# Performance work log

Measured on AMD Instinct MI355X. Metric: run time of the kernel, lower is better.

Reference implementation:

```python
import jax, jax.numpy as jnp
import numpy as np

N_LAYERS = 4
D_IN = 64
D_OUT = 64
D_MODEL = 512
D_STATE = 256
RMIN, RMAX, MAX_PHASE = 0.8, 0.95, 2.0 * np.pi


def setup_inputs() -> dict:
    key = jax.random.key(0)
    rng = np.random.default_rng(0)
    B, L = 8, 2048
    u = jax.random.normal(key, (B, L, D_IN), dtype=jnp.float32)
    # encoder/decoder (nn.Linear, bias=False): weight shape [out, in]
    encoder_w = jnp.asarray(rng.standard_normal((D_MODEL, D_IN)) / np.sqrt(D_IN), jnp.float32)
    decoder_w = jnp.asarray(rng.standard_normal((D_OUT, D_MODEL)) / np.sqrt(D_MODEL), jnp.float32)
    # LRU params per block (standard ring init on eigenvalues)
    u1 = rng.uniform(size=(N_LAYERS, D_STATE))
    u2 = rng.uniform(size=(N_LAYERS, D_STATE))
    nu_log = jnp.asarray(np.log(-0.5 * np.log(u1 * (RMAX**2 - RMIN**2) + RMIN**2)), jnp.float32)
    theta_log = jnp.asarray(np.log(MAX_PHASE * u2), jnp.float32)
    B_re = jnp.asarray(rng.standard_normal((N_LAYERS, D_STATE, D_MODEL)) / np.sqrt(2 * D_MODEL), jnp.float32)
    B_im = jnp.asarray(rng.standard_normal((N_LAYERS, D_STATE, D_MODEL)) / np.sqrt(2 * D_MODEL), jnp.float32)
    C_re = jnp.asarray(rng.standard_normal((N_LAYERS, D_MODEL, D_STATE)) / np.sqrt(D_STATE), jnp.float32)
    C_im = jnp.asarray(rng.standard_normal((N_LAYERS, D_MODEL, D_STATE)) / np.sqrt(D_STATE), jnp.float32)
    D = jnp.asarray(rng.standard_normal((N_LAYERS, D_MODEL)), jnp.float32)
    # GLU feedforward: y = (x W1^T) * sigmoid(x W2^T)
    W1 = jnp.asarray(rng.standard_normal((N_LAYERS, D_MODEL, D_MODEL)) / np.sqrt(D_MODEL), jnp.float32)
    W2 = jnp.asarray(rng.standard_normal((N_LAYERS, D_MODEL, D_MODEL)) / np.sqrt(D_MODEL), jnp.float32)
    res_logit = jnp.full((N_LAYERS,), -1.0, jnp.float32)
    return dict(u=u, encoder_w=encoder_w, decoder_w=decoder_w, nu_log=nu_log,
                theta_log=theta_log, B_re=B_re, B_im=B_im, C_re=C_re, C_im=C_im,
                D=D, W1=W1, W2=W2, res_logit=res_logit)


def _lru(x, nu, th, Bre, Bim, Cre, Cim, Dv):
    # diagonal complex LRU: h_t = lam*h_{t-1} + gamma*B u_t ; y = Re(C h) + D*u
    lam = jnp.exp(-jnp.exp(nu) + 1j * jnp.exp(th)).astype(jnp.complex64)  # [N]
    gam = jnp.sqrt(1.0 - jnp.abs(lam) ** 2).astype(jnp.complex64)
    Bc = (Bre + 1j * Bim).astype(jnp.complex64)  # [N, D]
    Bu = jnp.einsum('bld,nd->bln', x.astype(jnp.complex64), Bc) * gam  # [B,L,N]
    lam_b = jnp.broadcast_to(lam, Bu.shape)

    def comb(a, b):
        return (a[0] * b[0], a[1] * b[0] + b[1])

    _, h = jax.lax.associative_scan(comb, (lam_b, Bu), axis=1)
    Cc = (Cre + 1j * Cim).astype(jnp.complex64)  # [D, N]
    return jnp.real(jnp.einsum('bln,dn->bld', h, Cc)) + Dv * x


def reference(u, encoder_w, decoder_w, nu_log, theta_log, B_re, B_im, C_re, C_im, D, W1, W2, res_logit):
    x = jnp.einsum('bli,mi->blm', u, encoder_w)  # encoder
    for k in range(N_LAYERS):
        z = _lru(x, nu_log[k], theta_log[k], B_re[k], B_im[k], C_re[k], C_im[k], D[k])
        z = jnp.einsum('bld,od->blo', z, W1[k]) * jax.nn.sigmoid(jnp.einsum('bld,od->blo', z, W2[k]))
        x = x + jax.nn.sigmoid(res_logit[k]) * z  # gated residual (dropout=0)
    return jnp.einsum('blm,om->blo', x, decoder_w)  # decoder
```

## Files before the change

kernel.cpp:

```cpp
#include <hip/hip_runtime.h>
#include <cmath>

#define DM 512
#define DS 256
#define NL 4
#define BATCH 8
#define SEQ 2048
#define MROWS (BATCH*SEQ)
#define LCH 32
#define NCH 64

typedef unsigned short ushort_t;
typedef unsigned int uint_t;
typedef __attribute__((ext_vector_type(8))) short short8;
typedef __attribute__((ext_vector_type(4))) float floatx4;

__device__ __forceinline__ float sigmoidf_(float v) { return 1.0f / (1.0f + __expf(-v)); }

__device__ __forceinline__ ushort_t f2bf(float f) {
    union { float f; unsigned int u; } c; c.f = f;
    unsigned int u = c.u;
    u += 0x7fffu + ((u >> 16) & 1u);
    return (ushort_t)(u >> 16);
}
__device__ __forceinline__ float bf2f(uint_t h) {
    union { unsigned int u; float f; } c; c.u = (h & 0xffffu) << 16; return c.f;
}
__device__ __forceinline__ uint_t pack2(float a, float b) {
    return (uint_t)f2bf(a) | ((uint_t)f2bf(b) << 16);
}

#define AS1 __attribute__((address_space(1)))
#define AS3 __attribute__((address_space(3)))
__device__ __forceinline__ void gl_lds16(const void* g, void* l) {
    __builtin_amdgcn_global_load_lds((const AS1 uint_t*)g, (AS3 uint_t*)l, 16, 0, 0);
}

struct GemmArgs {
    const ushort_t* A;
    const ushort_t* Wa;
    const ushort_t* Wb;
    const ushort_t* xbf_in;
    const float* gam;
    const float* Dv;
    float* of32;
    ushort_t* obf;
    const float* resp;
    const float* lamre;
    const float* lamim;
    float* carry;
    int K;
    int N;
    int layer;
};

#define PREFETCH_TILE(it_, buf_)                                                        \
    do {                                                                                \
        const size_t kb_ = (size_t)(it_) * 64;                                          \
        char* dst_ = smem + (buf_) * HALF;                                              \
        gl_lds16(Ap + (size_t)(wid * 16 + lrow) * Kb + kb_, dst_ + wid * 1024);         \
        gl_lds16(Ap + (size_t)((wid + 4) * 16 + lrow) * Kb + kb_,                       \
                 dst_ + (wid + 4) * 1024);                                              \
        gl_lds16(B0p + (size_t)(wid * 16 + lrow) * Kb + kb_, dst_ + AB + wid * 1024);   \
        if constexpr (BN == 128) {                                                      \
            gl_lds16(B0p + (size_t)((wid + 4) * 16 + lrow) * Kb + kb_,                  \
                     dst_ + AB + (wid + 4) * 1024);                                     \
        }                                                                               \
        if constexpr (DUAL) {                                                           \
            gl_lds16(B1p + (size_t)(wid * 16 + lrow) * Kb + kb_,                        \
                     dst_ + AB + BB + wid * 1024);                                      \
            if constexpr (BN == 128) {                                                  \
                gl_lds16(B1p + (size_t)((wid + 4) * 16 + lrow) * Kb + kb_,              \
                         dst_ + AB + BB + (wid + 4) * 1024);                            \
            }                                                                           \
        }                                                                               \
    } while (0)

template<int BN, int EPI, int DUAL>
__launch_bounds__(256, DUAL ? 2 : 3)
__global__ void mgemm(const GemmArgs p) {
    constexpr int BM = 128;
    constexpr int MT = (BN == 128) ? 4 : 2;
    constexpr int NT = 4;
    constexpr int WROWS = MT * 16;
    constexpr int AB = 8192;
    constexpr int BB = (BN == 128) ? 8192 : 4096;
    constexpr int B1B = DUAL ? BB : 0;
    constexpr int HALF = AB + BB + B1B;
    constexpr int EPB = (EPI == 4) ? 0
                      : (EPI == 1) ? (32 * 132 * 4 + 128 * 66 * 4)
                      : 32 * 132 * 4;
    constexpr int SMB = (2 * HALF > EPB) ? 2 * HALF : EPB;
    __shared__ __align__(16) char smem[SMB];

    const int K = p.K, N = p.N;
    const int tid = threadIdx.x, lane = tid & 63, wid = tid >> 6;
    const int wm = (BN == 128) ? (wid & 1) : wid;
    const int wn = (BN == 128) ? (wid >> 1) : 0;
    const int m0 = blockIdx.x * BM, n0 = blockIdx.y * BN;
    const int q = lane >> 4, r16 = lane & 15;
    const int lrow = lane >> 2;
    const size_t Kb = (size_t)K * 2;
    const char* Ap  = (const char*)p.A  + (size_t)m0 * Kb + (lane & 3) * 16;
    const char* B0p = (const char*)p.Wa + (size_t)n0 * Kb + (lane & 3) * 16;
    const char* B1p = (const char*)p.Wb + (size_t)n0 * Kb + (lane & 3) * 16;

    floatx4 acc0[MT][NT] = {};
    floatx4 acc1[DUAL ? MT : 1][DUAL ? NT : 1] = {};

    const int iters = K >> 5;
    PREFETCH_TILE(0, 0);
    for (int it = 0; it < iters; ++it) {
        __syncthreads();
        if (it + 1 < iters) PREFETCH_TILE(it + 1, (it + 1) & 1);
        const ushort_t* As  = (const ushort_t*)(smem + (it & 1) * HALF);
        const ushort_t* Bs0 = (const ushort_t*)(smem + (it & 1) * HALF + AB);
        const ushort_t* Bs1 = (const ushort_t*)(smem + (it & 1) * HALF + AB + BB);

        short8 af[MT], b0[NT], b1[DUAL ? NT : 1];
#pragma unroll
        for (int i = 0; i < MT; ++i)
            af[i] = *(const short8*)&As[(wm * WROWS + i * 16 + r16) * 32 + q * 8];
#pragma unroll
        for (int j = 0; j < NT; ++j) {
            b0[j] = *(const short8*)&Bs0[(wn * 64 + j * 16 + r16) * 32 + q * 8];
            if constexpr (DUAL)
                b1[j] = *(const short8*)&Bs1[(wn * 64 + j * 16 + r16) * 32 + q * 8];
        }
#pragma unroll
        for (int i = 0; i < MT; ++i)
#pragma unroll
            for (int j = 0; j < NT; ++j) {
                acc0[i][j] = __builtin_amdgcn_mfma_f32_16x16x32_bf16(af[i], b0[j], acc0[i][j], 0, 0, 0);
                if constexpr (DUAL)
                    acc1[i][j] = __builtin_amdgcn_mfma_f32_16x16x32_bf16(af[i], b1[j], acc1[i][j], 0, 0, 0);
            }
    }

    if constexpr (EPI == 4) {
#pragma unroll
        for (int i = 0; i < MT; ++i)
#pragma unroll
            for (int j = 0; j < NT; ++j)
#pragma unroll
                for (int rr = 0; rr < 4; ++rr) {
                    const int row = m0 + wm * WROWS + i * 16 + q * 4 + rr;
                    const int col = wn * 64 + j * 16 + r16;
                    p.of32[(size_t)row * N + col] = acc0[i][j][rr];
                }
        return;
    } else {
        float* eps = (float*)smem;
        uint_t* zst = (uint_t*)(smem + 32 * 132 * 4);
        float rsv = 0.f;
        if constexpr (EPI == 3) rsv = sigmoidf_(p.resp[p.layer]);

#pragma unroll
        for (int i = 0; i < MT; ++i) {
            __syncthreads();
#pragma unroll
            for (int j = 0; j < NT; ++j) {
                const int colt = wn * 64 + j * 16 + r16;
#pragma unroll
                for (int rr = 0; rr < 4; ++rr) {
                    float v = acc0[i][j][rr];
                    if constexpr (EPI == 1) v *= p.gam[(n0 + colt) >> 1];
                    if constexpr (EPI == 3) v = rsv * v * sigmoidf_(acc1[i][j][rr]);
                    eps[(wm * 16 + q * 4 + rr) * 132 + colt] = v;
                }
            }
            __syncthreads();
            const int row_r = tid >> 3, colg = (tid & 7) * 16;
            const int lr = (row_r >> 4) * 64 + i * 16 + (row_r & 15);
            const int grow = m0 + lr;
            const int gcol = n0 + colg;
            float4 f[4];
#pragma unroll
            for (int c = 0; c < 4; ++c) f[c] = *(float4*)&eps[row_r * 132 + colg + c * 4];
            const size_t ob = (size_t)grow * N + gcol;

            if constexpr (EPI == 2) {
                uint_t xp[8];
                *(uint4*)(xp)     = *(const uint4*)(p.xbf_in + ob);
                *(uint4*)(xp + 4) = *(const uint4*)(p.xbf_in + ob + 8);
#pragma unroll
                for (int c = 0; c < 4; ++c) {
                    float4 dv = *(const float4*)(p.Dv + gcol + c * 4);
                    f[c].x += dv.x * bf2f(xp[2 * c]);
                    f[c].y += dv.y * bf2f(xp[2 * c] >> 16);
                    f[c].z += dv.z * bf2f(xp[2 * c + 1]);
                    f[c].w += dv.w * bf2f(xp[2 * c + 1] >> 16);
                }
            } else if constexpr (EPI == 3) {
                uint_t xp[8];
                *(uint4*)(xp)     = *(const uint4*)(p.xbf_in + ob);
                *(uint4*)(xp + 4) = *(const uint4*)(p.xbf_in + ob + 8);
#pragma unroll
                for (int c = 0; c < 4; ++c) {
                    f[c].x += bf2f(xp[2 * c]);
                    f[c].y += bf2f(xp[2 * c] >> 16);
                    f[c].z += bf2f(xp[2 * c + 1]);
                    f[c].w += bf2f(xp[2 * c + 1] >> 16);
                }
            }
            uint4 p0, p1;
            p0.x = pack2(f[0].x, f[0].y); p0.y = pack2(f[0].z, f[0].w);
            p0.z = pack2(f[1].x, f[1].y); p0.w = pack2(f[1].z, f[1].w);
            p1.x = pack2(f[2].x, f[2].y); p1.y = pack2(f[2].z, f[2].w);
            p1.z = pack2(f[3].x, f[3].y); p1.w = pack2(f[3].z, f[3].w);
            *(uint4*)(p.obf + ob) = p0;
            *(uint4*)(p.obf + ob + 8) = p1;
            if constexpr (EPI == 1) {
                const int c0 = colg >> 1;
                *(uint4*)&zst[lr * 66 + c0]     = p0;
                *(uint4*)&zst[lr * 66 + c0 + 4] = p1;
            }
        }

        if constexpr (EPI == 1) {
            __syncthreads();
            const int c4 = tid >> 6, s6 = tid & 63;
            const int sg = (n0 >> 1) + s6;
            const float lr_ = p.lamre[sg], li_ = p.lamim[sg];
            float hr = 0.f, hi = 0.f;
#pragma unroll 8
            for (int i2 = 0; i2 < LCH; ++i2) {
                uint_t uu = zst[(c4 * LCH + i2) * 66 + s6];
                float br = bf2f(uu), bi = bf2f(uu >> 16);
                float nr = fmaf(lr_, hr, fmaf(-li_, hi, br));
                float ni = fmaf(lr_, hi, fmaf(li_, hr, bi));
                hr = nr; hi = ni;
            }
            const int b = m0 >> 11;
            const int cblk = ((m0 & (SEQ - 1)) >> 5) + c4;
            const size_t cb = (size_t)(b * NCH + cblk) * 512 + sg;
            p.carry[cb] = hr; p.carry[cb + DS] = hi;
        }
    }
}

__global__ void prep_all(const float* __restrict__ u, const float* __restrict__ enc,
                         const float* __restrict__ dec, const float* __restrict__ nu,
                         const float* __restrict__ th,
                         const float* __restrict__ Bre, const float* __restrict__ Bim,
                         const float* __restrict__ Cre, const float* __restrict__ Cim,
                         const float* __restrict__ W1, const float* __restrict__ W2,
                         ushort_t* __restrict__ WBb, ushort_t* __restrict__ Wzb,
                         ushort_t* __restrict__ W1b, ushort_t* __restrict__ W2b,
                         ushort_t* __restrict__ encb, ushort_t* __restrict__ decb,
                         ushort_t* __restrict__ ubf,
                         float* __restrict__ lre, float* __restrict__ lim,
                         float* __restrict__ gm) {
    const int idx = blockIdx.x * 256 + threadIdx.x;
    const int k = idx & 511, n = (idx >> 9) & 511, l = idx >> 18;
    {
        const int s = n >> 1, part = n & 1;
        const float* src = part ? Bim : Bre;
        WBb[idx] = f2bf(src[((size_t)l * DS + s) * DM + k]);
    }
    {
        const int s = k >> 1, part = k & 1;
        float v = part ? -Cim[((size_t)l * DM + n) * DS + s]
                       :  Cre[((size_t)l * DM + n) * DS + s];
        Wzb[idx] = f2bf(v);
    }
    W1b[idx] = f2bf(W1[idx]);
    W2b[idx] = f2bf(W2[idx]);
    ubf[idx] = f2bf(u[idx]);
    if (idx < DM * 64) { encb[idx] = f2bf(enc[idx]); decb[idx] = f2bf(dec[idx]); }
    if (idx < NL * DS) {
        float a = expf(-expf(nu[idx])), t = expf(th[idx]);
        lre[idx] = a * cosf(t);
        lim[idx] = a * sinf(t);
        gm[idx] = sqrtf(fmaxf(0.f, 1.f - a * a));
    }
}

__global__ __launch_bounds__(256) void scan_apply_lb(
        const uint_t* __restrict__ Bu, const float* __restrict__ lre_,
        const float* __restrict__ lim_, const float* __restrict__ carry,
        uint_t* __restrict__ h) {
    const int s = threadIdx.x;
    const int blk = blockIdx.x, b = blk >> 6, c = blk & 63;
    const float lre = lre_[s], lim = lim_[s];

    float gre = 0.f, gim = 0.f;
    if (c > 0) {
        float are = lre, aim = lim;
#pragma unroll
        for (int t = 0; t < 5; ++t) {
            float nr = are * are - aim * aim, ni = 2.f * are * aim;
            are = nr; aim = ni;
        }
        const int depth = (c < 12) ? c : 12;
        float pwr = 1.f, pwi = 0.f;
        for (int j = c - 1; j >= c - depth; --j) {
            const size_t jb = (size_t)(b * NCH + j) * 512 + s;
            float er = carry[jb], ei = carry[jb + DS];
            gre = fmaf(pwr, er, fmaf(-pwi, ei, gre));
            gim = fmaf(pwr, ei, fmaf(pwi, er, gim));
            float nr = pwr * are - pwi * aim, ni = pwr * aim + pwi * are;
            pwr = nr; pwi = ni;
        }
    }

    float hr = gre, hi = gim;
    size_t base = ((size_t)b * SEQ + (size_t)c * LCH) * DS + s;
#pragma unroll 8
    for (int i = 0; i < LCH; ++i, base += DS) {
        uint_t uu = Bu[base];
        float br = bf2f(uu), bi = bf2f(uu >> 16);
        float nr = fmaf(lre, hr, fmaf(-lim, hi, br));
        float ni = fmaf(lre, hi, fmaf(lim, hr, bi));
        hr = nr; hi = ni;
        h[base] = pack2(hr, hi);
    }
}

extern "C" void kernel_launch(void* const* d_in, const int* in_sizes, int n_in,
                              void* d_out, int out_size, void* d_ws, size_t ws_size,
                              hipStream_t stream) {
    const float* u   = (const float*)d_in[0];
    const float* enc = (const float*)d_in[1];
    const float* dec = (const float*)d_in[2];
    const float* nu  = (const float*)d_in[3];
    const float* th  = (const float*)d_in[4];
    const float* Bre = (const float*)d_in[5];
    const float* Bim = (const float*)d_in[6];
    const float* Cre = (const float*)d_in[7];
    const float* Cim = (const float*)d_in[8];
    const float* Dp  = (const float*)d_in[9];
    const float* W1  = (const float*)d_in[10];
    const float* W2  = (const float*)d_in[11];
    const float* res = (const float*)d_in[12];
    float* out = (float*)d_out;

    const size_t MD = (size_t)MROWS * DM;
    float* carry = (float*)d_ws;
    float* lre  = carry + (size_t)BATCH * NCH * 512;
    float* lim  = lre + NL * DS;
    float* gmt  = lim + NL * DS;
    ushort_t* xbf  = (ushort_t*)(gmt + NL * DS);
    ushort_t* Bubf = xbf + MD;
    ushort_t* hbf  = Bubf + MD;
    ushort_t* zbf  = hbf + MD;
    ushort_t* ubf  = zbf;
    ushort_t* WBb  = zbf + MD;
    ushort_t* Wzb  = WBb + (size_t)NL * DM * DM;
    ushort_t* W1b  = Wzb + (size_t)NL * DM * DM;
    ushort_t* W2b  = W1b + (size_t)NL * DM * DM;
    ushort_t* encb = W2b + (size_t)NL * DM * DM;
    ushort_t* decb = encb + DM * 64;

    prep_all<<<NL * DM * DM / 256, 256, 0, stream>>>(
        u, enc, dec, nu, th, Bre, Bim, Cre, Cim, W1, W2,
        WBb, Wzb, W1b, W2b, encb, decb, ubf, lre, lim, gmt);

    const dim3 gFull(MROWS / 128, DM / 128);

    {
        GemmArgs a = {};
        a.A = ubf; a.Wa = encb; a.K = 64; a.N = DM;
        a.obf = xbf;
        mgemm<128, 0, 0><<<gFull, 256, 0, stream>>>(a);
    }

    for (int k = 0; k < NL; ++k) {
        {
            GemmArgs a = {};
            a.A = xbf; a.Wa = WBb + (size_t)k * DM * DM; a.K = DM; a.N = DM;
            a.obf = Bubf; a.gam = gmt + k * DS;
            a.lamre = lre + k * DS; a.lamim = lim + k * DS; a.carry = carry;
            mgemm<128, 1, 0><<<gFull, 256, 0, stream>>>(a);
        }
        scan_apply_lb<<<BATCH * NCH, 256, 0, stream>>>((const uint_t*)Bubf,
                                                       lre + k * DS, lim + k * DS, carry,
                                                       (uint_t*)hbf);
        {
            GemmArgs a = {};
            a.A = hbf; a.Wa = Wzb + (size_t)k * DM * DM; a.K = DM; a.N = DM;
            a.obf = zbf; a.xbf_in = xbf; a.Dv = Dp + k * DM;
            mgemm<128, 2, 0><<<gFull, 256, 0, stream>>>(a);
        }
        {
            GemmArgs a = {};
            a.A = zbf; a.Wa = W1b + (size_t)k * DM * DM; a.Wb = W2b + (size_t)k * DM * DM;
            a.K = DM; a.N = DM;
            a.obf = xbf; a.xbf_in = xbf; a.resp = res; a.layer = k;
            mgemm<128, 3, 1><<<gFull, 256, 0, stream>>>(a);
        }
    }
    {
        GemmArgs a = {};
        a.A = xbf; a.Wa = decb; a.K = DM; a.N = 64;
        a.of32 = out;
        mgemm<64, 4, 0><<<dim3(MROWS / 128, 1), 256, 0, stream>>>(a);
    }
}
```

Before: 369.6 us.

## Use 8-wave 512-thread blocks for 128x128 GEMM tiles, split decoder GEMM

The main GEMM kernel now runs 512 threads (8 waves) per 128x128 output tile, and each wave computes a 64x32 sub-tile instead of 64x64. Each wave issues one async tile load per matrix per K step, and the epilogue stages 64 rows per round in two rounds. More waves per tile are meant to hide latency better and to cut per-wave register pressure, which also raises occupancy for the dual-weight GLU variant. The decoder GEMM moves to its own 256-thread kernel. The trade-offs are higher LDS use for the epilogue staging and more barrier synchronisation across eight waves.

```diff
diff --git a/kernel.cpp b/kernel.cpp
--- a/kernel.cpp
+++ b/kernel.cpp
@@ -54,65 +54,48 @@
     int layer;
 };
 
-#define PREFETCH_TILE(it_, buf_)                                                        \
-    do {                                                                                \
-        const size_t kb_ = (size_t)(it_) * 64;                                          \
-        char* dst_ = smem + (buf_) * HALF;                                              \
-        gl_lds16(Ap + (size_t)(wid * 16 + lrow) * Kb + kb_, dst_ + wid * 1024);         \
-        gl_lds16(Ap + (size_t)((wid + 4) * 16 + lrow) * Kb + kb_,                       \
-                 dst_ + (wid + 4) * 1024);                                              \
-        gl_lds16(B0p + (size_t)(wid * 16 + lrow) * Kb + kb_, dst_ + AB + wid * 1024);   \
-        if constexpr (BN == 128) {                                                      \
-            gl_lds16(B0p + (size_t)((wid + 4) * 16 + lrow) * Kb + kb_,                  \
-                     dst_ + AB + (wid + 4) * 1024);                                     \
-        }                                                                               \
-        if constexpr (DUAL) {                                                           \
-            gl_lds16(B1p + (size_t)(wid * 16 + lrow) * Kb + kb_,                        \
-                     dst_ + AB + BB + wid * 1024);                                      \
-            if constexpr (BN == 128) {                                                  \
-                gl_lds16(B1p + (size_t)((wid + 4) * 16 + lrow) * Kb + kb_,              \
-                         dst_ + AB + BB + (wid + 4) * 1024);                            \
-            }                                                                           \
-        }                                                                               \
-    } while (0)
-
-template<int BN, int EPI, int DUAL>
-__launch_bounds__(256, DUAL ? 2 : 3)
-__global__ void mgemm(const GemmArgs p) {
+template<int EPI, int DUAL>
+__launch_bounds__(512, 4)
+__global__ void mgemm8(const GemmArgs p) {
     constexpr int BM = 128;
-    constexpr int MT = (BN == 128) ? 4 : 2;
-    constexpr int NT = 4;
-    constexpr int WROWS = MT * 16;
+    constexpr int MT = 4;
+    constexpr int NT = 2;
     constexpr int AB = 8192;
-    constexpr int BB = (BN == 128) ? 8192 : 4096;
+    constexpr int BB = 8192;
     constexpr int B1B = DUAL ? BB : 0;
     constexpr int HALF = AB + BB + B1B;
-    constexpr int EPB = (EPI == 4) ? 0
-                      : (EPI == 1) ? (32 * 132 * 4 + 128 * 66 * 4)
-                      : 32 * 132 * 4;
+    constexpr int EPB = (EPI == 1) ? (64 * 132 * 4 + 128 * 66 * 4) : 64 * 132 * 4;
     constexpr int SMB = (2 * HALF > EPB) ? 2 * HALF : EPB;
     __shared__ __align__(16) char smem[SMB];
 
     const int K = p.K, N = p.N;
     const int tid = threadIdx.x, lane = tid & 63, wid = tid >> 6;
-    const int wm = (BN == 128) ? (wid & 1) : wid;
-    const int wn = (BN == 128) ? (wid >> 1) : 0;
-    const int m0 = blockIdx.x * BM, n0 = blockIdx.y * BN;
+    const int wm = wid & 1, wn = wid >> 1;
+    const int m0 = blockIdx.x * BM, n0 = blockIdx.y * 128;
     const int q = lane >> 4, r16 = lane & 15;
     const int lrow = lane >> 2;
     const size_t Kb = (size_t)K * 2;
-    const char* Ap  = (const char*)p.A  + (size_t)m0 * Kb + (lane & 3) * 16;
-    const char* B0p = (const char*)p.Wa + (size_t)n0 * Kb + (lane & 3) * 16;
-    const char* B1p = (const char*)p.Wb + (size_t)n0 * Kb + (lane & 3) * 16;
+    const char* Ap  = (const char*)p.A  + (size_t)(m0 + wid * 16 + lrow) * Kb + (lane & 3) * 16;
+    const char* B0p = (const char*)p.Wa + (size_t)(n0 + wid * 16 + lrow) * Kb + (lane & 3) * 16;
+    const char* B1p = (const char*)p.Wb + (size_t)(n0 + wid * 16 + lrow) * Kb + (lane & 3) * 16;
 
     floatx4 acc0[MT][NT] = {};
     floatx4 acc1[DUAL ? MT : 1][DUAL ? NT : 1] = {};
 
+#define PF8(it_, buf_)                                                   \
+    do {                                                                 \
+        const size_t kb_ = (size_t)(it_) * 64;                           \
+        char* dst_ = smem + (buf_) * HALF + wid * 1024;                  \
+        gl_lds16(Ap + kb_, dst_);                                        \
+        gl_lds16(B0p + kb_, dst_ + AB);                                  \
+        if constexpr (DUAL) gl_lds16(B1p + kb_, dst_ + AB + BB);         \
+    } while (0)
+
     const int iters = K >> 5;
-    PREFETCH_TILE(0, 0);
+    PF8(0, 0);
     for (int it = 0; it < iters; ++it) {
         __syncthreads();
-        if (it + 1 < iters) PREFETCH_TILE(it + 1, (it + 1) & 1);
+        if (it + 1 < iters) PF8(it + 1, (it + 1) & 1);
         const ushort_t* As  = (const ushort_t*)(smem + (it & 1) * HALF);
         const ushort_t* Bs0 = (const ushort_t*)(smem + (it & 1) * HALF + AB);
         const ushort_t* Bs1 = (const ushort_t*)(smem + (it & 1) * HALF + AB + BB);
@@ -120,12 +103,12 @@
         short8 af[MT], b0[NT], b1[DUAL ? NT : 1];
 #pragma unroll
         for (int i = 0; i < MT; ++i)
-            af[i] = *(const short8*)&As[(wm * WROWS + i * 16 + r16) * 32 + q * 8];
+            af[i] = *(const short8*)&As[(wm * 64 + i * 16 + r16) * 32 + q * 8];
 #pragma unroll
         for (int j = 0; j < NT; ++j) {
-            b0[j] = *(const short8*)&Bs0[(wn * 64 + j * 16 + r16) * 32 + q * 8];
+            b0[j] = *(const short8*)&Bs0[(wn * 32 + j * 16 + r16) * 32 + q * 8];
             if constexpr (DUAL)
-                b1[j] = *(const short8*)&Bs1[(wn * 64 + j * 16 + r16) * 32 + q * 8];
+                b1[j] = *(const short8*)&Bs1[(wn * 32 + j * 16 + r16) * 32 + q * 8];
         }
 #pragma unroll
         for (int i = 0; i < MT; ++i)
@@ -136,89 +119,81 @@
                     acc1[i][j] = __builtin_amdgcn_mfma_f32_16x16x32_bf16(af[i], b1[j], acc1[i][j], 0, 0, 0);
             }
     }
-
-    if constexpr (EPI == 4) {
-#pragma unroll
-        for (int i = 0; i < MT; ++i)
-#pragma unroll
-            for (int j = 0; j < NT; ++j)
+#undef PF8
+
+    float* eps = (float*)smem;
+    uint_t* zst = (uint_t*)(smem + 64 * 132 * 4);
+    float rsv = 0.f;
+    if constexpr (EPI == 3) rsv = sigmoidf_(p.resp[p.layer]);
+
+#pragma unroll
+    for (int r = 0; r < 2; ++r) {
+        __syncthreads();
+#pragma unroll
+        for (int ii = 0; ii < 2; ++ii) {
+#pragma unroll
+            for (int j = 0; j < NT; ++j) {
+                const int colt = wn * 32 + j * 16 + r16;
 #pragma unroll
                 for (int rr = 0; rr < 4; ++rr) {
-                    const int row = m0 + wm * WROWS + i * 16 + q * 4 + rr;
-                    const int col = wn * 64 + j * 16 + r16;
-                    p.of32[(size_t)row * N + col] = acc0[i][j][rr];
+                    float v = acc0[r * 2 + ii][j][rr];
+                    if constexpr (EPI == 1) v *= p.gam[(n0 + colt) >> 1];
+                    if constexpr (EPI == 3) v = rsv * v * sigmoidf_(acc1[r * 2 + ii][j][rr]);
+                    eps[(wm * 32 + ii * 16 + q * 4 + rr) * 132 + colt] = v;
                 }
-        return;
-    } else {
-        float* eps = (float*)smem;
-        uint_t* zst = (uint_t*)(smem + 32 * 132 * 4);
-        float rsv = 0.f;
-        if constexpr (EPI == 3) rsv = sigmoidf_(p.resp[p.layer]);
-
-#pragma unroll
-        for (int i = 0; i < MT; ++i) {
-            __syncthreads();
-#pragma unroll
-            for (int j = 0; j < NT; ++j) {
-                const int colt = wn * 64 + j * 16 + r16;
-#pragma unroll
-                for (int rr = 0; rr < 4; ++rr) {
-                    float v = acc0[i][j][rr];
-                    if constexpr (EPI == 1) v *= p.gam[(n0 + colt) >> 1];
-                    if constexpr (EPI == 3) v = rsv * v * sigmoidf_(acc1[i][j][rr]);
-                    eps[(wm * 16 + q * 4 + rr) * 132 + colt] = v;
-                }
-            }
-            __syncthreads();
-            const int row_r = tid >> 3, colg = (tid & 7) * 16;
-            const int lr = (row_r >> 4) * 64 + i * 16 + (row_r & 15);
-            const int grow = m0 + lr;
-            const int gcol = n0 + colg;
-            float4 f[4];
-#pragma unroll
-            for (int c = 0; c < 4; ++c) f[c] = *(float4*)&eps[row_r * 132 + colg + c * 4];
-            const size_t ob = (size_t)grow * N + gcol;
-
-            if constexpr (EPI == 2) {
-                uint_t xp[8];
-                *(uint4*)(xp)     = *(const uint4*)(p.xbf_in + ob);
-                *(uint4*)(xp + 4) = *(const uint4*)(p.xbf_in + ob + 8);
-#pragma unroll
-                for (int c = 0; c < 4; ++c) {
-                    float4 dv = *(const float4*)(p.Dv + gcol + c * 4);
-                    f[c].x += dv.x * bf2f(xp[2 * c]);
-                    f[c].y += dv.y * bf2f(xp[2 * c] >> 16);
-                    f[c].z += dv.z * bf2f(xp[2 * c + 1]);
-                    f[c].w += dv.w * bf2f(xp[2 * c + 1] >> 16);
-                }
-            } else if constexpr (EPI == 3) {
-                uint_t xp[8];
-                *(uint4*)(xp)     = *(const uint4*)(p.xbf_in + ob);
-                *(uint4*)(xp + 4) = *(const uint4*)(p.xbf_in + ob + 8);
-#pragma unroll
-                for (int c = 0; c < 4; ++c) {
-                    f[c].x += bf2f(xp[2 * c]);
-                    f[c].y += bf2f(xp[2 * c] >> 16);
-                    f[c].z += bf2f(xp[2 * c + 1]);
-                    f[c].w += bf2f(xp[2 * c + 1] >> 16);
-                }
-            }
-            uint4 p0, p1;
-            p0.x = pack2(f[0].x, f[0].y); p0.y = pack2(f[0].z, f[0].w);
-            p0.z = pack2(f[1].x, f[1].y); p0.w = pack2(f[1].z, f[1].w);
-            p1.x = pack2(f[2].x, f[2].y); p1.y = pack2(f[2].z, f[2].w);
-            p1.z = pack2(f[3].x, f[3].y); p1.w = pack2(f[3].z, f[3].w);
-            *(uint4*)(p.obf + ob) = p0;
-            *(uint4*)(p.obf + ob + 8) = p1;
-            if constexpr (EPI == 1) {
-                const int c0 = colg >> 1;
-                *(uint4*)&zst[lr * 66 + c0]     = p0;
-                *(uint4*)&zst[lr * 66 + c0 + 4] = p1;
-            }
-        }
-
+            }
+        }
+        __syncthreads();
+        const int row_r = tid >> 3, colg = (tid & 7) * 16;
+        const int lr = (row_r >> 5) * 64 + r * 32 + ((row_r >> 4) & 1) * 16 + (row_r & 15);
+        const int grow = m0 + lr;
+        const int gcol = n0 + colg;
+        float4 f[4];
+#pragma unroll
+        for (int c = 0; c < 4; ++c) f[c] = *(float4*)&eps[row_r * 132 + colg + c * 4];
+        const size_t ob = (size_t)grow * N + gcol;
+
+        if constexpr (EPI == 2) {
+            uint_t xp[8];
+            *(uint4*)(xp)     = *(const uint4*)(p.xbf_in + ob);
+            *(uint4*)(xp + 4) = *(const uint4*)(p.xbf_in + ob + 8);
+#pragma unroll
+            for (int c = 0; c < 4; ++c) {
+                float4 dv = *(const float4*)(p.Dv + gcol + c * 4);
+                f[c].x += dv.x * bf2f(xp[2 * c]);
+                f[c].y += dv.y * bf2f(xp[2 * c] >> 16);
+                f[c].z += dv.z * bf2f(xp[2 * c + 1]);
+                f[c].w += dv.w * bf2f(xp[2 * c + 1] >> 16);
+            }
+        } else if constexpr (EPI == 3) {
+            uint_t xp[8];
+            *(uint4*)(xp)     = *(const uint4*)(p.xbf_in + ob);
+            *(uint4*)(xp + 4) = *(const uint4*)(p.xbf_in + ob + 8);
+#pragma unroll
+            for (int c = 0; c < 4; ++c) {
+                f[c].x += bf2f(xp[2 * c]);
+                f[c].y += bf2f(xp[2 * c] >> 16);
+                f[c].z += bf2f(xp[2 * c + 1]);
+                f[c].w += bf2f(xp[2 * c + 1] >> 16);
+            }
+        }
+        uint4 p0, p1;
+        p0.x = pack2(f[0].x, f[0].y); p0.y = pack2(f[0].z, f[0].w);
+        p0.z = pack2(f[1].x, f[1].y); p0.w = pack2(f[1].z, f[1].w);
+        p1.x = pack2(f[2].x, f[2].y); p1.y = pack2(f[2].z, f[2].w);
+        p1.z = pack2(f[3].x, f[3].y); p1.w = pack2(f[3].z, f[3].w);
+        *(uint4*)(p.obf + ob) = p0;
+        *(uint4*)(p.obf + ob + 8) = p1;
         if constexpr (EPI == 1) {
-            __syncthreads();
+            const int c0 = colg >> 1;
+            *(uint4*)&zst[lr * 66 + c0]     = p0;
+            *(uint4*)&zst[lr * 66 + c0 + 4] = p1;
+        }
+    }
+
+    if constexpr (EPI == 1) {
+        __syncthreads();
+        if (tid < 256) {
             const int c4 = tid >> 6, s6 = tid & 63;
             const int sg = (n0 >> 1) + s6;
             const float lr_ = p.lamre[sg], li_ = p.lamim[sg];
@@ -237,6 +212,70 @@
             p.carry[cb] = hr; p.carry[cb + DS] = hi;
         }
     }
+}
+
+__launch_bounds__(256, 3)
+__global__ void dgemm(const GemmArgs p) {
+    constexpr int MT = 2, NT = 4, WROWS = 32;
+    constexpr int AB = 8192, BB = 4096;
+    constexpr int HALF = AB + BB;
+    __shared__ __align__(16) char smem[2 * HALF];
+
+    const int K = p.K, N = p.N;
+    const int tid = threadIdx.x, lane = tid & 63, wid = tid >> 6;
+    const int wm = wid, wn = 0;
+    const int m0 = blockIdx.x * 128, n0 = 0;
+    const int q = lane >> 4, r16 = lane & 15;
+    const int lrow = lane >> 2;
+    const size_t Kb = (size_t)K * 2;
+    const char* Ap  = (const char*)p.A  + (size_t)m0 * Kb + (lane & 3) * 16;
+    const char* B0p = (const char*)p.Wa + (size_t)n0 * Kb + (lane & 3) * 16;
+
+    floatx4 acc0[MT][NT] = {};
+
+#define PFD(it_, buf_)                                                                  \
+    do {                                                                                \
+        const size_t kb_ = (size_t)(it_) * 64;                                          \
+        char* dst_ = smem + (buf_) * HALF;                                              \
+        gl_lds16(Ap + (size_t)(wid * 16 + lrow) * Kb + kb_, dst_ + wid * 1024);         \
+        gl_lds16(Ap + (size_t)((wid + 4) * 16 + lrow) * Kb + kb_,                       \
+                 dst_ + (wid + 4) * 1024);                                              \
+        gl_lds16(B0p + (size_t)(wid * 16 + lrow) * Kb + kb_, dst_ + AB + wid * 1024);   \
+    } while (0)
+
+    const int iters = K >> 5;
+    PFD(0, 0);
+    for (int it = 0; it < iters; ++it) {
+        __syncthreads();
+        if (it + 1 < iters) PFD(it + 1, (it + 1) & 1);
+        const ushort_t* As  = (const ushort_t*)(smem + (it & 1) * HALF);
+        const ushort_t* Bs0 = (const ushort_t*)(smem + (it & 1) * HALF + AB);
+
+        short8 af[MT], b0[NT];
+#pragma unroll
+        for (int i = 0; i < MT; ++i)
+            af[i] = *(const short8*)&As[(wm * WROWS + i * 16 + r16) * 32 + q * 8];
+#pragma unroll
+        for (int j = 0; j < NT; ++j)
+            b0[j] = *(const short8*)&Bs0[(wn * 64 + j * 16 + r16) * 32 + q * 8];
+#pragma unroll
+        for (int i = 0; i < MT; ++i)
+#pragma unroll
+            for (int j = 0; j < NT; ++j)
+                acc0[i][j] = __builtin_amdgcn_mfma_f32_16x16x32_bf16(af[i], b0[j], acc0[i][j], 0, 0, 0);
+    }
+#undef PFD
+
+#pragma unroll
+    for (int i = 0; i < MT; ++i)
+#pragma unroll
+        for (int j = 0; j < NT; ++j)
+#pragma unroll
+            for (int rr = 0; rr < 4; ++rr) {
+                const int row = m0 + wm * WROWS + i * 16 + q * 4 + rr;
+                const int col = wn * 64 + j * 16 + r16;
+                p.of32[(size_t)row * N + col] = acc0[i][j][rr];
+            }
 }
 
 __global__ void prep_all(const float* __restrict__ u, const float* __restrict__ enc,
@@ -362,7 +401,7 @@
         GemmArgs a = {};
         a.A = ubf; a.Wa = encb; a.K = 64; a.N = DM;
         a.obf = xbf;
-        mgemm<128, 0, 0><<<gFull, 256, 0, stream>>>(a);
+        mgemm8<0, 0><<<gFull, 512, 0, stream>>>(a);
     }
 
     for (int k = 0; k < NL; ++k) {
@@ -371,7 +410,7 @@
             a.A = xbf; a.Wa = WBb + (size_t)k * DM * DM; a.K = DM; a.N = DM;
             a.obf = Bubf; a.gam = gmt + k * DS;
             a.lamre = lre + k * DS; a.lamim = lim + k * DS; a.carry = carry;
-            mgemm<128, 1, 0><<<gFull, 256, 0, stream>>>(a);
+            mgemm8<1, 0><<<gFull, 512, 0, stream>>>(a);
         }
         scan_apply_lb<<<BATCH * NCH, 256, 0, stream>>>((const uint_t*)Bubf,
                                                        lre + k * DS, lim + k * DS, carry,
@@ -380,20 +419,20 @@
             GemmArgs a = {};
             a.A = hbf; a.Wa = Wzb + (size_t)k * DM * DM; a.K = DM; a.N = DM;
             a.obf = zbf; a.xbf_in = xbf; a.Dv = Dp + k * DM;
-            mgemm<128, 2, 0><<<gFull, 256, 0, stream>>>(a);
+            mgemm8<2, 0><<<gFull, 512, 0, stream>>>(a);
         }
         {
             GemmArgs a = {};
             a.A = zbf; a.Wa = W1b + (size_t)k * DM * DM; a.Wb = W2b + (size_t)k * DM * DM;
             a.K = DM; a.N = DM;
             a.obf = xbf; a.xbf_in = xbf; a.resp = res; a.layer = k;
-            mgemm<128, 3, 1><<<gFull, 256, 0, stream>>>(a);
+            mgemm8<3, 1><<<gFull, 512, 0, stream>>>(a);
         }
     }
     {
         GemmArgs a = {};
         a.A = xbf; a.Wa = decb; a.K = DM; a.N = 64;
         a.of32 = out;
-        mgemm<64, 4, 0><<<dim3(MROWS / 128, 1), 256, 0, stream>>>(a);
-    }
-}
+        dgemm<<<dim3(MROWS / 128, 1), 256, 0, stream>>>(a);
+    }
+}
```

New measurement: 369.7 us. No clear change (+0.0%).
